# Kernel tuning notes

Measured on AMD Instinct MI355X. Metric: run time of the kernel, lower is better.

The kernel has to match this reference:

```python
import jax, jax.numpy as jnp
import numpy as np

B = 64        # image batch
K = 8         # beam width k
T = 12        # program_len
H = 2048      # hd_sz
IN = 2048     # CNN feature size (in_sz)
D = 400       # num_draws (grammar size)
E = 128       # input_op_sz


def gumbel_log_survival(x):
    # log P(Gumbel > x), numerically stable (Kool et al.)
    y = jnp.exp(-x)
    return jnp.where(x >= 10.0, -x - y / 2 + y * y / 24,
                     jnp.log(-jnp.expm1(-jnp.exp(-jnp.minimum(x, 10.0)))))


def setup_inputs():
    key = jax.random.key(0)
    ks = jax.random.split(key, 14)
    s = lambda n: 1.0 / np.sqrt(n)
    f32 = jnp.float32
    return {
        "x_f": jax.random.normal(ks[0], (B, IN), f32),
        "x_f3_seq": jax.random.normal(ks[1], (T, B * K, IN), f32),
        "gumbel_u": jax.random.uniform(ks[2], (T, B * K, D), dtype=f32),
        "pop_syms": jax.random.randint(ks[3], (T, B * K), 0, D),
        "mask_table": jnp.where(jax.random.uniform(ks[4], (D, D)) < 0.25, -20.0, 0.0).astype(f32),
        "W_emb": jax.random.normal(ks[5], (E, D), f32) * s(D),
        "b_emb": jnp.zeros((E,), f32),
        "W_ih": jax.random.normal(ks[6], (4 * H, 2 * IN + E), f32) * s(2 * IN + E),
        "W_hh": jax.random.normal(ks[7], (4 * H, H), f32) * s(H),
        "b_ih": jnp.zeros((4 * H,), f32),
        "b_hh": jnp.zeros((4 * H,), f32),
        "W_fc1": jax.random.normal(ks[8], (H, H), f32) * s(H),
        "b_fc1": jnp.zeros((H,), f32),
        "W_out": jax.random.normal(ks[9], (D, H), f32) * s(H),
        "b_out": jnp.zeros((D,), f32),
    }


def _forward(x_f, x_f3_seq, gumbel_u, mask_table, W_emb, b_emb, W_ih, W_hh,
             b_ih, b_hh, W_fc1, b_fc1, W_out, b_out, pop_syms):
    BK = B * K
    sg = jax.lax.stop_gradient
    xf = jnp.tile(x_f, (K, 1))                        # [BK, IN] beams share CNN feature
    mask_bin = (mask_table == 0).astype(jnp.float32)  # mask.get_mask
    rows = jnp.arange(BK)
    base = jnp.tile(jnp.arange(B), K)
    bias = b_ih + b_hh

    def step(carry, xs):
        h, c, G, logp, samples, outs, ent, entp, wpq, lgp = carry
        t, pop, xf3, u = xs
        # one-hot(pop) -> dense+relu op embedding
        emb = jax.nn.relu(jax.nn.one_hot(pop, D, dtype=jnp.float32) @ W_emb.T + b_emb)
        # single-step LSTM (torch gate order i,f,g,o); dropout is identity (eval)
        z = jnp.concatenate([xf, emb, xf3], axis=1) @ W_ih.T + h @ W_hh.T + bias
        i_, f_, g_, o_ = jnp.split(z, 4, axis=-1)
        c2 = jax.nn.sigmoid(f_) * c + jax.nn.sigmoid(i_) * jnp.tanh(g_)
        h2 = jax.nn.sigmoid(o_) * jnp.tanh(c2)
        hd = jax.nn.relu(h2 @ W_fc1.T + b_fc1)
        logits = hd @ W_out.T + b_out + mask_table[pop]
        logp_tok = jax.nn.log_softmax(logits, axis=1)
        probs = jnp.exp(logp_tok)
        greedy = jnp.argmax(probs, axis=1)

        # Gumbel-with-maximum + top-k beam step (all detached, as in torch)
        gum = -jnp.log(-jnp.log(jnp.clip(u, 1e-9, 1.0 - 1e-9)))
        g_phi = sg(logp_tok) + sg(logp) + gum
        Z = jnp.max(g_phi, axis=1, keepdims=True)
        v = G - g_phi + jnp.log1p(-jnp.exp(g_phi - Z))
        g = sg(G - jax.nn.relu(v) - jnp.log1p(jnp.exp(-jnp.abs(v))))
        # beams are laid out in blocks of B rows; gather per-image candidates
        g2 = g.reshape(K, B, D).transpose(1, 0, 2).reshape(B, K * D)
        g_val, idx = jax.lax.top_k(g2, K)
        is0 = t == 0
        order = jnp.where(is0, rows, (idx // D).T.reshape(BK) * B + base)
        sample = jnp.where(is0, greedy, (idx % D).T.reshape(BK))
        G2 = jnp.where(is0, G, g_val.T.reshape(BK, 1))

        out_lp = logp_tok[order]
        out_pr = probs[order]
        sel = jnp.take_along_axis(out_lp, sample[:, None], axis=1)  # [BK,1]
        logp2 = jnp.where(is0, logp[order], logp[order] + sel)
        samples2 = samples[order].at[:, t].set(sample.astype(jnp.float32))
        outs2 = outs[order].at[:, t].set(sel[:, 0])

        # importance-weighted entropy estimate (active for t > 0)
        ent_full = jnp.sum(out_lp * out_pr * mask_bin[pop[order]], axis=1)
        g_k = sg(jnp.tile(g_val[:, -1:], (1, K - 1)))
        phi_k = logp2[:, 0].reshape(K, B).T[:, :K - 1]
        w = sg(jnp.exp(phi_k - gumbel_log_survival(g_k - sg(phi_k))))
        ent_mat = ent_full.reshape(K, B).T[:, :K - 1]
        upd = jnp.sum(w * ent_mat, axis=1)
        ent2 = ent + jnp.where(is0, 0.0, upd / jnp.sum(w, axis=1))
        entp2 = entp + jnp.where(is0, 0.0, upd)
        wpq2 = jnp.where(is0, wpq, w)
        lgp2 = jnp.where(is0, lgp, phi_k)
        new_carry = (h2[order], c2[order], G2, logp2, samples2, outs2,
                     ent2, entp2, wpq2, lgp2)
        return new_carry, None

    f32 = jnp.float32
    carry0 = (jnp.zeros((BK, H), f32), jnp.zeros((BK, H), f32),
              jnp.zeros((BK, 1), f32), jnp.zeros((BK, 1), f32),
              jnp.zeros((BK, T), f32), jnp.zeros((BK, T), f32),
              jnp.zeros((B,), f32), jnp.zeros((B,), f32),
              jnp.zeros((B, K - 1), f32), jnp.zeros((B, K - 1), f32))
    xs = (jnp.arange(T), pop_syms, x_f3_seq, gumbel_u)
    (_, _, _, _, samples, outs, ent, entp, wpq, lgp), _ = jax.lax.scan(step, carry0, xs)
    # drop last beam, lay out [B, (K-1)*T] as in the torch split/cat epilogue
    take = lambda a: a.reshape(K, B, T)[:K - 1].transpose(1, 0, 2).reshape(B, (K - 1) * T)
    return take(outs), take(samples), ent, wpq, lgp


def reference(x_f, x_f3_seq, gumbel_u, pop_syms, mask_table, W_emb, b_emb, W_ih,
              W_hh, b_ih, b_hh, W_fc1, b_fc1, W_out, b_out):
    return _forward(x_f, x_f3_seq, gumbel_u, mask_table, W_emb, b_emb, W_ih, W_hh,
                    b_ih, b_hh, W_fc1, b_fc1, W_out, b_out, pop_syms)
```

## Files before the change

### kernel.cpp

```cpp
#include <hip/hip_runtime.h>
#include <math.h>


#define BB   64
#define KK   8
#define TT   12
#define HH   2048
#define DD   400
#define EE   128
#define BKR  512
#define G4   8192

static const size_t OFF_STATE = 0;
static const size_t OFF_H     = 114688;
static const size_t OFF_C     = 4308992;
static const size_t ZERO_END  = 8503296;
static const size_t OFF_Z     = 8503296;
static const size_t OFF_H2    = 42057728;
static const size_t OFF_C2    = 46252032;
static const size_t OFF_HD    = 50446336;
static const size_t OFF_EMB   = 54640640;
static const size_t OFF_XFW   = 54902784;
static const size_t OFF_BIAS  = 56999936;
static const size_t OFF_LPT   = 57032704;
static const size_t OFF_GMAT  = 58671104;
static const size_t OFF_INTS  = 60309504;
static const size_t WS_TOTAL  = 60313600;

#define SI_G    0
#define SI_LOGP 512
#define SI_SAMP 1024
#define SI_OUTS 7168
#define SI_ENT  13312
#define SI_WPQ  13376
#define SI_LGP  13824

using half8  = __attribute__((ext_vector_type(8))) _Float16;
using floatx4 = __attribute__((ext_vector_type(4))) float;

__global__ __launch_bounds__(256, 2)
void ij_gemm_f16x3(const float* __restrict__ A0, const float* __restrict__ A1,
                   const float* __restrict__ A2, int kA1, int kA2,
                   int lda0, int lda1, int lda2,
                   const float* __restrict__ B0, const float* __restrict__ B1,
                   int kB1, int ldb0, int ldb1,
                   float* __restrict__ C, int N, int Klen)
{
    __shared__ half8 lds[2048];

    const int tid = threadIdx.x;
    const int n0  = blockIdx.x * 128;
    const int m0  = blockIdx.y * 128;
    const int kstart = blockIdx.z * Klen;
    const int nch = Klen / 32;
    float* Cout = C + (size_t)blockIdx.z * ((size_t)512 * (size_t)N);

    const int wid    = tid >> 6;
    const int wave_m = wid & 1;
    const int wave_n = wid >> 1;
    const int lane   = tid & 63;
    const int lo16   = lane & 15;
    const int oq     = lane >> 4;
    const int laneSlot = oq * 16 + ((lo16 + 4 * oq) & 15);

    const int st_o   = tid & 3;
    const int st_row0 = tid >> 2;
    const int st_slot = ((st_row0 & 15) + 4 * st_o) & 15;

    float4 pfA[2][2], pfB[2][2];

    auto loadGlobals = [&](int c) {
        const int kb = kstart + c * 32;
#pragma unroll
        for (int i = 0; i < 2; ++i) {
            const int row = st_row0 + i * 64;
            const int kc  = kb + st_o * 8;
            const float* ap; int ao, ld;
            if (kc < kA1)      { ap = A0; ao = kc;       ld = lda0; }
            else if (kc < kA2) { ap = A1; ao = kc - kA1; ld = lda1; }
            else               { ap = A2; ao = kc - kA2; ld = lda2; }
            const float* p = ap + (size_t)(m0 + row) * ld + ao;
            pfA[i][0] = *(const float4*)(p);
            pfA[i][1] = *(const float4*)(p + 4);
            const int bn = n0 + row;
            const float* bp; int bo, bld;
            if (kc < kB1) { bp = B0; bo = kc;       bld = ldb0; }
            else          { bp = B1; bo = kc - kB1; bld = ldb1; }
            if (bn < N) {
                const float* q = bp + (size_t)bn * bld + bo;
                pfB[i][0] = *(const float4*)(q);
                pfB[i][1] = *(const float4*)(q + 4);
            } else {
                pfB[i][0] = make_float4(0.f,0.f,0.f,0.f);
                pfB[i][1] = make_float4(0.f,0.f,0.f,0.f);
            }
        }
    };

    auto writeLDS = [&]() {
#pragma unroll
        for (int i = 0; i < 2; ++i) {
            const int row = st_row0 + i * 64;
            const int mt  = row >> 4;
            const int idx = mt * 64 + st_o * 16 + (((row & 15) + 4 * st_o) & 15);
            {
                float x[8] = {pfA[i][0].x, pfA[i][0].y, pfA[i][0].z, pfA[i][0].w,
                              pfA[i][1].x, pfA[i][1].y, pfA[i][1].z, pfA[i][1].w};
                half8 hi8, lo8;
#pragma unroll
                for (int j = 0; j < 8; ++j) {
                    _Float16 h = (_Float16)x[j];
                    hi8[j] = h;
                    lo8[j] = (_Float16)((x[j] - (float)h) * 2048.0f);
                }
                lds[idx]       = hi8;
                lds[512 + idx] = lo8;
            }
            {
                float x[8] = {pfB[i][0].x, pfB[i][0].y, pfB[i][0].z, pfB[i][0].w,
                              pfB[i][1].x, pfB[i][1].y, pfB[i][1].z, pfB[i][1].w};
                half8 hi8, lo8;
#pragma unroll
                for (int j = 0; j < 8; ++j) {
                    _Float16 h = (_Float16)x[j];
                    hi8[j] = h;
                    lo8[j] = (_Float16)((x[j] - (float)h) * 2048.0f);
                }
                lds[1024 + idx] = hi8;
                lds[1536 + idx] = lo8;
            }
        }
    };

    floatx4 acc1[4][4], acc2[4][4];
#pragma unroll
    for (int i = 0; i < 4; ++i)
#pragma unroll
        for (int j = 0; j < 4; ++j) { acc1[i][j] = (floatx4)0.f; acc2[i][j] = (floatx4)0.f; }

    loadGlobals(0);
    for (int c = 0; c < nch; ++c) {
        __syncthreads();
        writeLDS();
        __syncthreads();
        if (c + 1 < nch) loadGlobals(c + 1);

        half8 Ahi[4], Alo[4];
#pragma unroll
        for (int mt = 0; mt < 4; ++mt) {
            const int amt = wave_m * 4 + mt;
            Ahi[mt] = lds[amt * 64 + laneSlot];
            Alo[mt] = lds[512 + amt * 64 + laneSlot];
        }
#pragma unroll
        for (int nt = 0; nt < 4; ++nt) {
            const int bnt = wave_n * 4 + nt;
            half8 Bhi = lds[1024 + bnt * 64 + laneSlot];
            half8 Blo = lds[1536 + bnt * 64 + laneSlot];
#pragma unroll
            for (int mt = 0; mt < 4; ++mt) {
                acc1[mt][nt] = __builtin_amdgcn_mfma_f32_16x16x32_f16(Ahi[mt], Bhi, acc1[mt][nt], 0, 0, 0);
                acc2[mt][nt] = __builtin_amdgcn_mfma_f32_16x16x32_f16(Ahi[mt], Blo, acc2[mt][nt], 0, 0, 0);
                acc2[mt][nt] = __builtin_amdgcn_mfma_f32_16x16x32_f16(Alo[mt], Bhi, acc2[mt][nt], 0, 0, 0);
            }
        }
    }

    const float s = 1.0f / 2048.0f;
#pragma unroll
    for (int mt = 0; mt < 4; ++mt) {
        const int rbase = m0 + wave_m * 64 + mt * 16 + oq * 4;
#pragma unroll
        for (int nt = 0; nt < 4; ++nt) {
            const int col = n0 + wave_n * 64 + nt * 16 + lo16;
            if (col >= N) continue;
#pragma unroll
            for (int v = 0; v < 4; ++v) {
                float val = acc1[mt][nt][v] + acc2[mt][nt][v] * s;
                Cout[(size_t)(rbase + v) * N + col] = val;
            }
        }
    }
}

#define FBM 128
#define FBN 64
#define FBK 16

__global__ __launch_bounds__(256, 2)
void ij_gemm_f32(const float* __restrict__ A0, const float* __restrict__ A1,
                 const float* __restrict__ A2, int kA1, int kA2,
                 int lda0, int lda1, int lda2,
                 const float* __restrict__ B0, const float* __restrict__ B1,
                 int kB1, int ldb0, int ldb1,
                 float* __restrict__ C, int M, int N, int Klen)
{
    __shared__ float As[2][FBK][FBM];
    __shared__ float Bs[2][FBK][FBN];

    const int tid = threadIdx.x;
    const int tx  = tid & 15;
    const int ty  = tid >> 4;
    const int n0  = blockIdx.x * FBN;
    const int m0  = blockIdx.y * FBM;
    const int kstart = blockIdx.z * Klen;
    const int nch = Klen / FBK;
    float* Cout = C + (size_t)blockIdx.z * ((size_t)M * (size_t)N);

    const int srow = tid >> 2;
    const int kq   = tid & 3;

    float4 aR0, aR1, bR;

    auto loadChunk = [&](int kb0) {
        const int kc = kb0 + kq * 4;
        const float* ap; int ao, ld;
        if (kc < kA1)      { ap = A0; ao = kc;       ld = lda0; }
        else if (kc < kA2) { ap = A1; ao = kc - kA1; ld = lda1; }
        else               { ap = A2; ao = kc - kA2; ld = lda2; }
        const int r0 = m0 + srow, r1 = r0 + 64;
        aR0 = (r0 < M) ? *(const float4*)(ap + (size_t)r0 * ld + ao)
                       : make_float4(0.f, 0.f, 0.f, 0.f);
        aR1 = (r1 < M) ? *(const float4*)(ap + (size_t)r1 * ld + ao)
                       : make_float4(0.f, 0.f, 0.f, 0.f);
        const float* bp; int bo, bld;
        if (kc < kB1) { bp = B0; bo = kc;       bld = ldb0; }
        else          { bp = B1; bo = kc - kB1; bld = ldb1; }
        const int bn = n0 + srow;
        bR = (bn < N) ? *(const float4*)(bp + (size_t)bn * bld + bo)
                      : make_float4(0.f, 0.f, 0.f, 0.f);
    };
    auto storeChunk = [&](int bsel) {
        const int k4 = kq * 4;
        As[bsel][k4+0][srow]      = aR0.x;
        As[bsel][k4+1][srow]      = aR0.y;
        As[bsel][k4+2][srow]      = aR0.z;
        As[bsel][k4+3][srow]      = aR0.w;
        As[bsel][k4+0][srow + 64] = aR1.x;
        As[bsel][k4+1][srow + 64] = aR1.y;
        As[bsel][k4+2][srow + 64] = aR1.z;
        As[bsel][k4+3][srow + 64] = aR1.w;
        Bs[bsel][k4+0][srow]      = bR.x;
        Bs[bsel][k4+1][srow]      = bR.y;
        Bs[bsel][k4+2][srow]      = bR.z;
        Bs[bsel][k4+3][srow]      = bR.w;
    };

    float acc[8][4];
#pragma unroll
    for (int i = 0; i < 8; ++i)
#pragma unroll
        for (int j = 0; j < 4; ++j) acc[i][j] = 0.f;

    loadChunk(kstart);
    storeChunk(0);
    __syncthreads();
    int bsel = 0;
    for (int c = 0; c < nch; ++c) {
        if (c + 1 < nch) loadChunk(kstart + (c + 1) * FBK);
#pragma unroll
        for (int kkk = 0; kkk < FBK; ++kkk) {
            float a[8], b[4];
            const float4 av0 = *(const float4*)&As[bsel][kkk][ty * 8];
            const float4 av1 = *(const float4*)&As[bsel][kkk][ty * 8 + 4];
            a[0]=av0.x; a[1]=av0.y; a[2]=av0.z; a[3]=av0.w;
            a[4]=av1.x; a[5]=av1.y; a[6]=av1.z; a[7]=av1.w;
            const float2 bv0 = *(const float2*)&Bs[bsel][kkk][tx * 2];
            const float2 bv1 = *(const float2*)&Bs[bsel][kkk][tx * 2 + 32];
            b[0]=bv0.x; b[1]=bv0.y; b[2]=bv1.x; b[3]=bv1.y;
#pragma unroll
            for (int i = 0; i < 8; ++i)
#pragma unroll
                for (int j = 0; j < 4; ++j)
                    acc[i][j] = fmaf(a[i], b[j], acc[i][j]);
        }
        if (c + 1 < nch) storeChunk(bsel ^ 1);
        __syncthreads();
        bsel ^= 1;
    }

#pragma unroll
    for (int i = 0; i < 8; ++i) {
        const int row = m0 + ty * 8 + i;
        if (row >= M) continue;
        const size_t rbase = (size_t)row * N;
#pragma unroll
        for (int g = 0; g < 2; ++g) {
            const int col = n0 + tx * 2 + g * 32;
            if (col + 1 < N) {
                float2 st; st.x = acc[i][g*2+0]; st.y = acc[i][g*2+1];
                *(float2*)(Cout + rbase + col) = st;
            } else if (col < N) {
                Cout[rbase + col] = acc[i][g*2+0];
            }
        }
    }
}

__global__ void ij_bias_kernel(const float* __restrict__ b_ih, const float* __restrict__ b_hh,
                               float* __restrict__ bias)
{
    int i = blockIdx.x * 256 + threadIdx.x;
    if (i < G4) bias[i] = b_ih[i] + b_hh[i];
}

__global__ void ij_emb_kernel(const float* __restrict__ W_emb, const float* __restrict__ b_emb,
                              const int* __restrict__ pop_t, float* __restrict__ emb)
{
    int i = blockIdx.x * 256 + threadIdx.x;
    if (i >= BKR * EE) return;
    int r = i >> 7, e = i & 127;
    float v = W_emb[e * DD + pop_t[r]] + b_emb[e];
    emb[i] = v > 0.f ? v : 0.f;
}

__global__ void ij_lstm_kernel(const float* __restrict__ z0, const float* __restrict__ z1,
                               const float* __restrict__ xfw, const float* __restrict__ bias,
                               const float* __restrict__ c,
                               float* __restrict__ h2, float* __restrict__ c2)
{
    int i = blockIdx.x * 256 + threadIdx.x;
    if (i >= BKR * HH) return;
    int r = i >> 11, hh = i & 2047;
    const size_t zb = (size_t)r * G4;
    const float* xw = xfw + (size_t)(r & 63) * G4;
    float iv = z0[zb + hh]        + z1[zb + hh]        + xw[hh]        + bias[hh];
    float fv = z0[zb + HH + hh]   + z1[zb + HH + hh]   + xw[HH + hh]   + bias[HH + hh];
    float gv = z0[zb + 2*HH + hh] + z1[zb + 2*HH + hh] + xw[2*HH + hh] + bias[2*HH + hh];
    float ov = z0[zb + 3*HH + hh] + z1[zb + 3*HH + hh] + xw[3*HH + hh] + bias[3*HH + hh];
    float si = 1.f / (1.f + expf(-iv));
    float sf = 1.f / (1.f + expf(-fv));
    float so = 1.f / (1.f + expf(-ov));
    float cv = sf * c[i] + si * tanhf(gv);
    c2[i] = cv;
    h2[i] = so * tanhf(cv);
}

__global__ void ij_reduce_fc1_kernel(const float* __restrict__ part, const float* __restrict__ b_fc1,
                                     float* __restrict__ hd)
{
    int i = blockIdx.x * 256 + threadIdx.x;
    if (i >= BKR * HH) return;
    float v = part[i] + part[i + 1048576] + part[i + 2097152] + part[i + 3145728]
            + b_fc1[i & 2047];
    hd[i] = v > 0.f ? v : 0.f;
}

__global__ void ij_reduce_xfw_kernel(const float* __restrict__ part, float* __restrict__ xfw)
{
    int i = blockIdx.x * 256 + threadIdx.x;
    if (i >= BB * G4) return;
    xfw[i] = part[i] + part[i + 524288] + part[i + 1048576] + part[i + 1572864];
}

__global__ __launch_bounds__(256)
void ij_softmax_g_kernel(const float* __restrict__ part, const float* __restrict__ b_out,
                         const float* __restrict__ mask_table, const int* __restrict__ pop_t,
                         const float* __restrict__ gum_t, const double* __restrict__ G,
                         const double* __restrict__ logp,
                         double* __restrict__ logp_tok, double* __restrict__ gmat,
                         int* __restrict__ greedy)
{
    const int r = blockIdx.x, tid = threadIdx.x;
    __shared__ double sred[256];
    __shared__ int    sidx[256];
    __shared__ double sbc[2];

    const int pop = pop_t[r];
    const int j0 = tid, j1 = tid + 256;
    double lg0 = -INFINITY, lg1 = -INFINITY;
    if (j0 < DD) {
        double v = (double)b_out[j0] + (double)mask_table[pop * DD + j0];
#pragma unroll
        for (int s = 0; s < 16; ++s) v += (double)part[(size_t)s * (BKR*DD) + (size_t)r * DD + j0];
        lg0 = v;
    }
    if (j1 < DD) {
        double v = (double)b_out[j1] + (double)mask_table[pop * DD + j1];
#pragma unroll
        for (int s = 0; s < 16; ++s) v += (double)part[(size_t)s * (BKR*DD) + (size_t)r * DD + j1];
        lg1 = v;
    }
    double mv = lg0; int mi = j0;
    if (lg1 > mv) { mv = lg1; mi = j1; }
    sred[tid] = mv; sidx[tid] = mi;
    __syncthreads();
    for (int off = 128; off > 0; off >>= 1) {
        if (tid < off) {
            double ov = sred[tid+off]; int oi = sidx[tid+off];
            if (ov > sred[tid] || (ov == sred[tid] && oi < sidx[tid])) { sred[tid] = ov; sidx[tid] = oi; }
        }
        __syncthreads();
    }
    if (tid == 0) { sbc[0] = sred[0]; greedy[r] = sidx[0]; }
    __syncthreads();
    const double rowmax = sbc[0];

    double es = 0.0;
    if (j0 < DD) es += exp(lg0 - rowmax);
    if (j1 < DD) es += exp(lg1 - rowmax);
    __syncthreads();
    sred[tid] = es;
    __syncthreads();
    for (int off = 128; off > 0; off >>= 1) {
        if (tid < off) sred[tid] += sred[tid+off];
        __syncthreads();
    }
    if (tid == 0) sbc[1] = log(sred[0]);
    __syncthreads();
    const double lse = sbc[1];
    const double lpr = logp[r], Gr = G[r];

    double gp0 = -INFINITY, gp1 = -INFINITY;
    if (j0 < DD) {
        double lt = lg0 - rowmax - lse;
        logp_tok[(size_t)r * DD + j0] = lt;
        double u = (double)gum_t[(size_t)r * DD + j0];
        u = fmin(fmax(u, 1e-9), 1.0 - 1e-9);
        gp0 = lt + lpr + (-log(-log(u)));
    }
    if (j1 < DD) {
        double lt = lg1 - rowmax - lse;
        logp_tok[(size_t)r * DD + j1] = lt;
        double u = (double)gum_t[(size_t)r * DD + j1];
        u = fmin(fmax(u, 1e-9), 1.0 - 1e-9);
        gp1 = lt + lpr + (-log(-log(u)));
    }
    __syncthreads();
    sred[tid] = fmax(gp0, gp1);
    __syncthreads();
    for (int off = 128; off > 0; off >>= 1) {
        if (tid < off) sred[tid] = fmax(sred[tid], sred[tid+off]);
        __syncthreads();
    }
    const double Z = sred[0];
    if (j0 < DD) {
        double v = Gr - gp0 + log1p(-exp(gp0 - Z));
        gmat[(size_t)r * DD + j0] = Gr - fmax(v, 0.0) - log1p(exp(-fabs(v)));
    }
    if (j1 < DD) {
        double v = Gr - gp1 + log1p(-exp(gp1 - Z));
        gmat[(size_t)r * DD + j1] = Gr - fmax(v, 0.0) - log1p(exp(-fabs(v)));
    }
}

__global__ __launch_bounds__(256)
void ij_beam_kernel(const double* __restrict__ gmat, const double* __restrict__ logp_tok,
                    const int* __restrict__ greedy, const int* __restrict__ pop_t,
                    const float* __restrict__ mask_table,
                    double* __restrict__ G, double* __restrict__ logp,
                    double* __restrict__ samples, double* __restrict__ outs,
                    double* __restrict__ entacc, double* __restrict__ wpq,
                    double* __restrict__ lgp_o, int* __restrict__ order_g, int t)
{
    const int b = blockIdx.x, tid = threadIdx.x;
    __shared__ double sv[256];
    __shared__ int    si2[256];
    __shared__ double gval8[8];
    __shared__ int    gidx8[8];
    __shared__ int    ord8[8], smp8[8];
    __shared__ double lp28[8], sel8[8], Gn8[8];
    __shared__ double oldS[8][TT], oldO[8][TT];
    __shared__ double efull[8];

    if (t > 0) {
        for (int pass = 0; pass < 8; ++pass) {
            double bv = -INFINITY; int bi = 0x7fffffff;
            for (int cand = tid; cand < KK * DD; cand += 256) {
                bool used = false;
                for (int p = 0; p < pass; ++p) used |= (gidx8[p] == cand);
                if (used) continue;
                int kb2 = cand / DD, d = cand - kb2 * DD;
                double v = gmat[(size_t)(kb2 * BB + b) * DD + d];
                if (v > bv || (v == bv && cand < bi)) { bv = v; bi = cand; }
            }
            sv[tid] = bv; si2[tid] = bi;
            __syncthreads();
            for (int off = 128; off > 0; off >>= 1) {
                if (tid < off) {
                    double ov = sv[tid+off]; int oi = si2[tid+off];
                    if (ov > sv[tid] || (ov == sv[tid] && oi < si2[tid])) { sv[tid] = ov; si2[tid] = oi; }
                }
                __syncthreads();
            }
            if (tid == 0) { gval8[pass] = sv[0]; gidx8[pass] = si2[0]; }
            __syncthreads();
        }
    }

    if (tid < 8) {
        const int s = tid, rp = s * BB + b;
        int ord, smp; double Gn;
        if (t == 0) { ord = rp; smp = greedy[rp]; Gn = G[rp]; }
        else {
            int idx = gidx8[s]; int kb2 = idx / DD;
            ord = kb2 * BB + b; smp = idx - kb2 * DD; Gn = gval8[s];
        }
        ord8[s] = ord; smp8[s] = smp; Gn8[s] = Gn;
        double sel = logp_tok[(size_t)ord * DD + smp];
        double lp2 = (t == 0) ? logp[ord] : logp[ord] + sel;
        sel8[s] = sel; lp28[s] = lp2;
    }
    __syncthreads();
    if (tid < 8 * TT) {
        int s = tid / TT, ttc = tid - s * TT;
        oldS[s][ttc] = samples[ord8[s] * TT + ttc];
        oldO[s][ttc] = outs[ord8[s] * TT + ttc];
    }
    __syncthreads();
    if (tid < 8 * TT) {
        int s = tid / TT, ttc = tid - s * TT;
        int rp = s * BB + b;
        samples[rp * TT + ttc] = (ttc == t) ? (double)smp8[s] : oldS[s][ttc];
        outs[rp * TT + ttc]    = (ttc == t) ? sel8[s]         : oldO[s][ttc];
    }
    if (tid >= 96 && tid < 104) {
        int s = tid - 96, rp = s * BB + b;
        G[rp]       = Gn8[s];
        logp[rp]    = lp28[s];
        order_g[rp] = ord8[s];
    }

    if (t > 0) {
        for (int s = 0; s < KK - 1; ++s) {
            const int ord = ord8[s];
            const double* lrow = logp_tok + (size_t)ord * DD;
            const float*  mrow = mask_table + (size_t)pop_t[ord] * DD;
            double acc = 0.0;
            for (int j = tid; j < DD; j += 256) {
                double lp_ = lrow[j];
                if (mrow[j] == 0.0f) acc += lp_ * exp(lp_);
            }
            __syncthreads();
            sv[tid] = acc;
            __syncthreads();
            for (int off = 128; off > 0; off >>= 1) {
                if (tid < off) sv[tid] += sv[tid+off];
                __syncthreads();
            }
            if (tid == 0) efull[s] = sv[0];
            __syncthreads();
        }
        if (tid == 0) {
            const double gk = gval8[7];
            double sw = 0.0, swe = 0.0;
            for (int s = 0; s < KK - 1; ++s) {
                double phi = lp28[s];
                double x = gk - phi;
                double y = exp(-x);
                double gls;
                if (x >= 10.0) gls = -x - y * 0.5 + y * y * (1.0 / 24.0);
                else           gls = log(-expm1(-exp(-fmin(x, 10.0))));
                double w = exp(phi - gls);
                wpq[b * (KK-1) + s]   = w;
                lgp_o[b * (KK-1) + s] = phi;
                sw += w; swe += w * efull[s];
            }
            entacc[b] += swe / sw;
        }
    }
}

__global__ void ij_permute_kernel(const float* __restrict__ h2, const float* __restrict__ c2,
                                  const int* __restrict__ order_g,
                                  float* __restrict__ h, float* __restrict__ c)
{
    int i = blockIdx.x * 256 + threadIdx.x;
    if (i >= BKR * HH) return;
    int r = i >> 11, j = i & 2047;
    int o = order_g[r];
    h[i] = h2[(size_t)o * HH + j];
    c[i] = c2[(size_t)o * HH + j];
}

__global__ void ij_final_kernel(const double* __restrict__ outs, const double* __restrict__ samples,
                                const double* __restrict__ entacc, const double* __restrict__ wpq,
                                const double* __restrict__ lgp_o, float* __restrict__ out)
{
    int i = blockIdx.x * 256 + threadIdx.x;
    if (i < 5376) {
        int bb = i / 84, rest = i - bb * 84;
        int s = rest / TT, ttc = rest - s * TT;
        size_t src = (size_t)(s * BB + bb) * TT + ttc;
        out[i]        = (float)outs[src];
        out[5376 + i] = (float)samples[src];
    } else if (i < 5440) {
        out[10752 + (i - 5376)] = (float)entacc[i - 5376];
    } else if (i < 5888) {
        int q = i - 5440; out[10816 + q] = (float)wpq[q];
    } else if (i < 6336) {
        int q = i - 5888; out[11264 + q] = (float)lgp_o[q];
    }
}

extern "C" void kernel_launch(void* const* d_in, const int* in_sizes, int n_in,
                              void* d_out, int out_size, void* d_ws, size_t ws_size,
                              hipStream_t stream)
{
    const float* x_f   = (const float*)d_in[0];
    const float* x_f3  = (const float*)d_in[1];
    const float* gum   = (const float*)d_in[2];
    const int*   pop   = (const int*)d_in[3];
    const float* mask  = (const float*)d_in[4];
    const float* W_emb = (const float*)d_in[5];
    const float* b_emb = (const float*)d_in[6];
    const float* W_ih  = (const float*)d_in[7];
    const float* W_hh  = (const float*)d_in[8];
    const float* b_ih  = (const float*)d_in[9];
    const float* b_hh  = (const float*)d_in[10];
    const float* W_fc1 = (const float*)d_in[11];
    const float* b_fc1 = (const float*)d_in[12];
    const float* W_out = (const float*)d_in[13];
    const float* b_out = (const float*)d_in[14];
    float* out = (float*)d_out;
    char*  ws  = (char*)d_ws;

    if (ws_size < WS_TOTAL) return;

    double* STATE = (double*)(ws + OFF_STATE);
    double* Gv    = STATE + SI_G;
    double* LOGP  = STATE + SI_LOGP;
    double* SAMP  = STATE + SI_SAMP;
    double* OUTS  = STATE + SI_OUTS;
    double* ENT   = STATE + SI_ENT;
    double* WPQ   = STATE + SI_WPQ;
    double* LGP   = STATE + SI_LGP;
    float*  H     = (float*)(ws + OFF_H);
    float*  Cc    = (float*)(ws + OFF_C);
    float*  Z     = (float*)(ws + OFF_Z);
    float*  Z1    = Z + (size_t)BKR * G4;
    float*  H2    = (float*)(ws + OFF_H2);
    float*  C2    = (float*)(ws + OFF_C2);
    float*  HD    = (float*)(ws + OFF_HD);
    float*  EMB   = (float*)(ws + OFF_EMB);
    float*  XFW   = (float*)(ws + OFF_XFW);
    float*  BIAS  = (float*)(ws + OFF_BIAS);
    double* LPT   = (double*)(ws + OFF_LPT);
    double* GMAT  = (double*)(ws + OFF_GMAT);
    int*    ORDER = (int*)(ws + OFF_INTS);
    int*    GREEDY= ORDER + 512;

    hipMemsetAsync(ws, 0, ZERO_END, stream);
    ij_bias_kernel<<<32, 256, 0, stream>>>(b_ih, b_hh, BIAS);

    ij_gemm_f32<<<dim3(128, 1, 4), 256, 0, stream>>>(
        x_f, nullptr, nullptr, 1 << 30, 1 << 30, 2048, 0, 0,
        W_ih, nullptr, 1 << 30, 4224, 0,
        Z, BB, G4, 512);
    ij_reduce_xfw_kernel<<<2048, 256, 0, stream>>>(Z, XFW);

    for (int t = 0; t < TT; ++t) {
        const int* pop_t = pop + t * BKR;
        ij_emb_kernel<<<256, 256, 0, stream>>>(W_emb, b_emb, pop_t, EMB);

        ij_gemm_f16x3<<<dim3(64, 4, 2), 256, 0, stream>>>(
            EMB, x_f3 + (size_t)t * BKR * 2048, H, 128, 2176, 128, 2048, 2048,
            W_ih + 2048, W_hh, 2176, 4224, 2048,
            Z, G4, 2112);

        ij_lstm_kernel<<<4096, 256, 0, stream>>>(Z, Z1, XFW, BIAS, Cc, H2, C2);

        ij_gemm_f16x3<<<dim3(16, 4, 4), 256, 0, stream>>>(
            H2, nullptr, nullptr, 1 << 30, 1 << 30, 2048, 0, 0,
            W_fc1, nullptr, 1 << 30, 2048, 0,
            Z, HH, 512);
        ij_reduce_fc1_kernel<<<4096, 256, 0, stream>>>(Z, b_fc1, HD);

        ij_gemm_f16x3<<<dim3(4, 4, 16), 256, 0, stream>>>(
            HD, nullptr, nullptr, 1 << 30, 1 << 30, 2048, 0, 0,
            W_out, nullptr, 1 << 30, 2048, 0,
            Z, DD, 128);

        ij_softmax_g_kernel<<<512, 256, 0, stream>>>(
            Z, b_out, mask, pop_t, gum + (size_t)t * BKR * DD,
            Gv, LOGP, LPT, GMAT, GREEDY);

        ij_beam_kernel<<<64, 256, 0, stream>>>(
            GMAT, LPT, GREEDY, pop_t, mask,
            Gv, LOGP, SAMP, OUTS, ENT, WPQ, LGP, ORDER, t);

        ij_permute_kernel<<<4096, 256, 0, stream>>>(H2, C2, ORDER, H, Cc);
    }

    ij_final_kernel<<<25, 256, 0, stream>>>(OUTS, SAMP, ENT, WPQ, LGP, out);
    (void)in_sizes; (void)n_in; (void)out_size;
}
```

Measured before the change: 3.704 ms.

## Prepack fp16 hi/lo operands into MFMA tile layout and stream via LDS-direct loads

Adds a new execution path that converts the weights (W_ih, W_hh, W_fc1, W_out) and the per-step CNN features into split fp16 hi/lo pairs once per call. They are stored in a tiled layout that matches the MFMA fragment order. Producer kernels (embedding, LSTM cell, fc1 reduce, beam permute) now emit their outputs directly in this packed format. A new GEMM kernel then fills LDS with global_load_lds and does no per-tile fp32-to-fp16 splitting, removing conversion ALU work and register staging from the inner loop. In exchange, the path needs a much larger workspace and an up-front packing pass over all weights on every call, and it only runs when the provided workspace is big enough.

```diff
diff --git a/kernel.cpp b/kernel.cpp
--- a/kernel.cpp
+++ b/kernel.cpp
@@ -27,6 +27,27 @@
 static const size_t OFF_INTS  = 60309504;
 static const size_t WS_TOTAL  = 60313600;
 
+static const size_t NOFF_STATE = 0;
+static const size_t NOFF_C     = 114688;
+static const size_t NOFF_A16H  = 4308992;
+static const size_t NZERO_END  = 8503296;
+static const size_t NOFF_Z     = 8503296;
+static const size_t NOFF_H2    = 42057728;
+static const size_t NOFF_C2    = 46252032;
+static const size_t NOFF_XFW   = 50446336;
+static const size_t NOFF_BIAS  = 52543488;
+static const size_t NOFF_LPT   = 52576256;
+static const size_t NOFF_GMAT  = 54214656;
+static const size_t NOFF_INTS  = 55853056;
+static const size_t NOFF_A16E  = 55857152;
+static const size_t NOFF_A16X  = 56119296;
+static const size_t NOFF_A16F  = 106450944;
+static const size_t NOFF_A16D  = 110645248;
+static const size_t NOFF_B16G  = 114839552;
+static const size_t NOFF_B16F  = 253251584;
+static const size_t NOFF_B16O  = 270028800;
+static const size_t NWS_TOTAL  = 274223104;
+
 #define SI_G    0
 #define SI_LOGP 512
 #define SI_SAMP 1024
@@ -38,6 +59,300 @@
 using half8  = __attribute__((ext_vector_type(8))) _Float16;
 using floatx4 = __attribute__((ext_vector_type(4))) float;
 
+__device__ __forceinline__ void gload16(const void* g, void* l) {
+    __builtin_amdgcn_global_load_lds((__attribute__((address_space(1))) void*)g,
+                                     (__attribute__((address_space(3))) void*)l,
+                                     16, 0, 0);
+}
+
+__device__ __forceinline__ void split16v(float x, half8& hi, half8& lo, int j) {
+    _Float16 h = (_Float16)x;
+    hi[j] = h;
+    lo[j] = (_Float16)((x - (float)h) * 2048.0f);
+}
+
+__global__ __launch_bounds__(256, 2)
+void ij_gemm_pk(const half8* __restrict__ A0, const half8* __restrict__ A1,
+                const half8* __restrict__ A2, int cA1, int cA2,
+                int chA0, int chA1, int chA2,
+                const half8* __restrict__ Bt, int totB,
+                float* __restrict__ C, int N, int cpz)
+{
+    __shared__ half8 lds[2048];
+
+    const int tid  = threadIdx.x;
+    const int lane = tid & 63;
+    const int wid  = tid >> 6;
+    const int n0   = blockIdx.x * 128;
+    const int m0   = blockIdx.y * 128;
+    const int c0   = blockIdx.z * cpz;
+    float* Cout = C + (size_t)blockIdx.z * ((size_t)512 * (size_t)N);
+
+    const int wave_m = wid & 1;
+    const int wave_n = wid >> 1;
+    const int lo16 = lane & 15;
+    const int oq   = lane >> 4;
+
+    floatx4 acc1[4][4], acc2[4][4];
+#pragma unroll
+    for (int i = 0; i < 4; ++i)
+#pragma unroll
+        for (int j = 0; j < 4; ++j) { acc1[i][j] = (floatx4)0.f; acc2[i][j] = (floatx4)0.f; }
+
+    for (int c = 0; c < cpz; ++c) {
+        const int ca = c0 + c;
+        __syncthreads();
+        if (wid < 2) {
+            const half8* ap; int cl, st;
+            if (ca < cA1)      { ap = A0; cl = ca;       st = chA0; }
+            else if (ca < cA2) { ap = A1; cl = ca - cA1; st = chA1; }
+            else               { ap = A2; cl = ca - cA2; st = chA2; }
+            const half8* src = ap + ((size_t)blockIdx.y * st + cl) * 1024 + lane;
+#pragma unroll
+            for (int j = 0; j < 8; ++j) {
+                const int un = (wid * 8 + j) * 64;
+                gload16(src + un, &lds[un]);
+            }
+        } else {
+            const half8* src = Bt + ((size_t)blockIdx.x * totB + ca) * 1024 + lane;
+#pragma unroll
+            for (int j = 0; j < 8; ++j) {
+                const int un = ((wid - 2) * 8 + j) * 64;
+                gload16(src + un, &lds[1024 + un]);
+            }
+        }
+        __syncthreads();
+
+        half8 Ahi[4], Alo[4];
+#pragma unroll
+        for (int mt = 0; mt < 4; ++mt) {
+            const int amt = wave_m * 4 + mt;
+            Ahi[mt] = lds[amt * 64 + lane];
+            Alo[mt] = lds[512 + amt * 64 + lane];
+        }
+#pragma unroll
+        for (int nt = 0; nt < 4; ++nt) {
+            const int bnt = wave_n * 4 + nt;
+            half8 Bhi = lds[1024 + bnt * 64 + lane];
+            half8 Blo = lds[1536 + bnt * 64 + lane];
+#pragma unroll
+            for (int mt = 0; mt < 4; ++mt) {
+                acc1[mt][nt] = __builtin_amdgcn_mfma_f32_16x16x32_f16(Ahi[mt], Bhi, acc1[mt][nt], 0, 0, 0);
+                acc2[mt][nt] = __builtin_amdgcn_mfma_f32_16x16x32_f16(Ahi[mt], Blo, acc2[mt][nt], 0, 0, 0);
+                acc2[mt][nt] = __builtin_amdgcn_mfma_f32_16x16x32_f16(Alo[mt], Bhi, acc2[mt][nt], 0, 0, 0);
+            }
+        }
+    }
+
+    const float s = 1.0f / 2048.0f;
+#pragma unroll
+    for (int mt = 0; mt < 4; ++mt) {
+        const int rbase = m0 + wave_m * 64 + mt * 16 + oq * 4;
+#pragma unroll
+        for (int nt = 0; nt < 4; ++nt) {
+            const int col = n0 + wave_n * 64 + nt * 16 + lo16;
+            if (col >= N) continue;
+#pragma unroll
+            for (int v = 0; v < 4; ++v) {
+                float val = acc1[mt][nt][v] + acc2[mt][nt][v] * s;
+                Cout[(size_t)(rbase + v) * N + col] = val;
+            }
+        }
+    }
+}
+
+__global__ void ij_pack_w(const float* __restrict__ S0, const float* __restrict__ S1,
+                          int kS1, int ld0, int ld1,
+                          int Nw, int tot_ch, int total, half8* __restrict__ out)
+{
+    int gid = blockIdx.x * 256 + threadIdx.x;
+    if (gid >= total) return;
+    const int kpr  = tot_ch * 4;
+    const int koct = gid % kpr;
+    const int row  = gid / kpr;
+    const int c  = koct >> 2;
+    const int oqq = koct & 3;
+    const int k0 = koct * 8;
+    const int nb = row >> 7, mt = (row >> 4) & 7, lo16 = row & 15;
+    const int u  = mt * 64 + oqq * 16 + lo16;
+
+    half8 hi8, lo8;
+    if (row < Nw) {
+        const float* sp; int ko, ld;
+        if (k0 < kS1) { sp = S0; ko = k0;       ld = ld0; }
+        else          { sp = S1; ko = k0 - kS1; ld = ld1; }
+        const float4 a = *(const float4*)(sp + (size_t)row * ld + ko);
+        const float4 b = *(const float4*)(sp + (size_t)row * ld + ko + 4);
+        float x[8] = {a.x, a.y, a.z, a.w, b.x, b.y, b.z, b.w};
+#pragma unroll
+        for (int j = 0; j < 8; ++j) split16v(x[j], hi8, lo8, j);
+    } else {
+#pragma unroll
+        for (int j = 0; j < 8; ++j) { hi8[j] = (_Float16)0.f; lo8[j] = (_Float16)0.f; }
+    }
+    const size_t base = ((size_t)nb * tot_ch + c) * 1024;
+    out[base + u]       = hi8;
+    out[base + 512 + u] = lo8;
+}
+
+__global__ void ij_pack_emb(const float* __restrict__ W_emb, const float* __restrict__ b_emb,
+                            const int* __restrict__ pop_t, half8* __restrict__ out)
+{
+    int gid = blockIdx.x * 256 + threadIdx.x;
+    if (gid >= BKR * 16) return;
+    const int koct = gid & 15;
+    const int row  = gid >> 4;
+    const int c  = koct >> 2;
+    const int oqq = koct & 3;
+    const int k0 = koct * 8;
+    const int nb = row >> 7, mt = (row >> 4) & 7, lo16 = row & 15;
+    const int u  = mt * 64 + oqq * 16 + lo16;
+    const int p  = pop_t[row];
+
+    half8 hi8, lo8;
+#pragma unroll
+    for (int e = 0; e < 8; ++e) {
+        const int col = k0 + e;
+        float v = W_emb[col * DD + p] + b_emb[col];
+        v = v > 0.f ? v : 0.f;
+        split16v(v, hi8, lo8, e);
+    }
+    const size_t base = ((size_t)nb * 4 + c) * 1024;
+    out[base + u]       = hi8;
+    out[base + 512 + u] = lo8;
+}
+
+__global__ void ij_lstm_pk(const float* __restrict__ z0, const float* __restrict__ z1,
+                           const float* __restrict__ xfw, const float* __restrict__ bias,
+                           const float* __restrict__ c,
+                           float* __restrict__ h2, float* __restrict__ c2,
+                           half8* __restrict__ a16f)
+{
+    int gid = blockIdx.x * 256 + threadIdx.x;
+    if (gid >= BKR * 256) return;
+    const int r   = gid >> 8;
+    const int oct = gid & 255;
+    const int hh0 = oct * 8;
+    const size_t zb = (size_t)r * G4;
+    const float* xw = xfw + (size_t)(r & 63) * G4;
+
+    float zg[4][8];
+#pragma unroll
+    for (int g = 0; g < 4; ++g) {
+        const int base = g * HH + hh0;
+        const float4 a0 = *(const float4*)(z0 + zb + base);
+        const float4 a1 = *(const float4*)(z0 + zb + base + 4);
+        const float4 b0 = *(const float4*)(z1 + zb + base);
+        const float4 b1 = *(const float4*)(z1 + zb + base + 4);
+        const float4 w0 = *(const float4*)(xw + base);
+        const float4 w1 = *(const float4*)(xw + base + 4);
+        const float4 s0 = *(const float4*)(bias + base);
+        const float4 s1 = *(const float4*)(bias + base + 4);
+        zg[g][0] = a0.x + b0.x + w0.x + s0.x;  zg[g][1] = a0.y + b0.y + w0.y + s0.y;
+        zg[g][2] = a0.z + b0.z + w0.z + s0.z;  zg[g][3] = a0.w + b0.w + w0.w + s0.w;
+        zg[g][4] = a1.x + b1.x + w1.x + s1.x;  zg[g][5] = a1.y + b1.y + w1.y + s1.y;
+        zg[g][6] = a1.z + b1.z + w1.z + s1.z;  zg[g][7] = a1.w + b1.w + w1.w + s1.w;
+    }
+    const size_t ib = (size_t)r * HH + hh0;
+    const float4 cp0 = *(const float4*)(c + ib);
+    const float4 cp1 = *(const float4*)(c + ib + 4);
+    float cprev[8] = {cp0.x, cp0.y, cp0.z, cp0.w, cp1.x, cp1.y, cp1.z, cp1.w};
+
+    float h2v[8], c2v[8];
+#pragma unroll
+    for (int e = 0; e < 8; ++e) {
+        float si = 1.f / (1.f + expf(-zg[0][e]));
+        float sf = 1.f / (1.f + expf(-zg[1][e]));
+        float gt = tanhf(zg[2][e]);
+        float so = 1.f / (1.f + expf(-zg[3][e]));
+        float cv = sf * cprev[e] + si * gt;
+        c2v[e] = cv;
+        h2v[e] = so * tanhf(cv);
+    }
+    *(float4*)(c2 + ib)     = make_float4(c2v[0], c2v[1], c2v[2], c2v[3]);
+    *(float4*)(c2 + ib + 4) = make_float4(c2v[4], c2v[5], c2v[6], c2v[7]);
+    *(float4*)(h2 + ib)     = make_float4(h2v[0], h2v[1], h2v[2], h2v[3]);
+    *(float4*)(h2 + ib + 4) = make_float4(h2v[4], h2v[5], h2v[6], h2v[7]);
+
+    half8 hi8, lo8;
+#pragma unroll
+    for (int e = 0; e < 8; ++e) split16v(h2v[e], hi8, lo8, e);
+    const int cch = oct >> 2, oqq = oct & 3;
+    const int mt = (r >> 4) & 7, lo16 = r & 15;
+    const size_t base = ((size_t)(r >> 7) * 64 + cch) * 1024;
+    const int u = mt * 64 + oqq * 16 + lo16;
+    a16f[base + u]       = hi8;
+    a16f[base + 512 + u] = lo8;
+}
+
+__global__ void ij_reduce_fc1_pk(const float* __restrict__ part, const float* __restrict__ b_fc1,
+                                 half8* __restrict__ a16d)
+{
+    int gid = blockIdx.x * 256 + threadIdx.x;
+    if (gid >= BKR * 256) return;
+    const int r   = gid >> 8;
+    const int oct = gid & 255;
+    const int hh0 = oct * 8;
+    const size_t i = (size_t)r * HH + hh0;
+
+    float v[8];
+    {
+        const float4 b0 = *(const float4*)(b_fc1 + hh0);
+        const float4 b1 = *(const float4*)(b_fc1 + hh0 + 4);
+        v[0]=b0.x; v[1]=b0.y; v[2]=b0.z; v[3]=b0.w; v[4]=b1.x; v[5]=b1.y; v[6]=b1.z; v[7]=b1.w;
+    }
+#pragma unroll
+    for (int s = 0; s < 8; ++s) {
+        const float4 p0 = *(const float4*)(part + (size_t)s * 1048576 + i);
+        const float4 p1 = *(const float4*)(part + (size_t)s * 1048576 + i + 4);
+        v[0]+=p0.x; v[1]+=p0.y; v[2]+=p0.z; v[3]+=p0.w; v[4]+=p1.x; v[5]+=p1.y; v[6]+=p1.z; v[7]+=p1.w;
+    }
+    half8 hi8, lo8;
+#pragma unroll
+    for (int e = 0; e < 8; ++e) {
+        float x = v[e] > 0.f ? v[e] : 0.f;
+        split16v(x, hi8, lo8, e);
+    }
+    const int cch = oct >> 2, oqq = oct & 3;
+    const int mt = (r >> 4) & 7, lo16 = r & 15;
+    const size_t base = ((size_t)(r >> 7) * 64 + cch) * 1024;
+    const int u = mt * 64 + oqq * 16 + lo16;
+    a16d[base + u]       = hi8;
+    a16d[base + 512 + u] = lo8;
+}
+
+__global__ void ij_permute_pk(const float* __restrict__ h2, const float* __restrict__ c2,
+                              const int* __restrict__ order_g,
+                              float* __restrict__ c, half8* __restrict__ a16h)
+{
+    int gid = blockIdx.x * 256 + threadIdx.x;
+    if (gid >= BKR * 256) return;
+    const int r   = gid >> 8;
+    const int oct = gid & 255;
+    const int hh0 = oct * 8;
+    const int o   = order_g[r];
+    const size_t so_ = (size_t)o * HH + hh0;
+    const size_t di  = (size_t)r * HH + hh0;
+
+    const float4 cc0 = *(const float4*)(c2 + so_);
+    const float4 cc1 = *(const float4*)(c2 + so_ + 4);
+    *(float4*)(c + di)     = cc0;
+    *(float4*)(c + di + 4) = cc1;
+
+    const float4 hh0v = *(const float4*)(h2 + so_);
+    const float4 hh1v = *(const float4*)(h2 + so_ + 4);
+    float hv[8] = {hh0v.x, hh0v.y, hh0v.z, hh0v.w, hh1v.x, hh1v.y, hh1v.z, hh1v.w};
+    half8 hi8, lo8;
+#pragma unroll
+    for (int e = 0; e < 8; ++e) split16v(hv[e], hi8, lo8, e);
+    const int cch = oct >> 2, oqq = oct & 3;
+    const int mt = (r >> 4) & 7, lo16 = r & 15;
+    const size_t base = ((size_t)(r >> 7) * 64 + cch) * 1024;
+    const int u = mt * 64 + oqq * 16 + lo16;
+    a16h[base + u]       = hi8;
+    a16h[base + 512 + u] = lo8;
+}
+
 __global__ __launch_bounds__(256, 2)
 void ij_gemm_f16x3(const float* __restrict__ A0, const float* __restrict__ A1,
                    const float* __restrict__ A2, int kA1, int kA2,
@@ -65,7 +380,6 @@
 
     const int st_o   = tid & 3;
     const int st_row0 = tid >> 2;
-    const int st_slot = ((st_row0 & 15) + 4 * st_o) & 15;
 
     float4 pfA[2][2], pfB[2][2];
 
@@ -108,11 +422,7 @@
                               pfA[i][1].x, pfA[i][1].y, pfA[i][1].z, pfA[i][1].w};
                 half8 hi8, lo8;
 #pragma unroll
-                for (int j = 0; j < 8; ++j) {
-                    _Float16 h = (_Float16)x[j];
-                    hi8[j] = h;
-                    lo8[j] = (_Float16)((x[j] - (float)h) * 2048.0f);
-                }
+                for (int j = 0; j < 8; ++j) split16v(x[j], hi8, lo8, j);
                 lds[idx]       = hi8;
                 lds[512 + idx] = lo8;
             }
@@ -121,11 +431,7 @@
                               pfB[i][1].x, pfB[i][1].y, pfB[i][1].z, pfB[i][1].w};
                 half8 hi8, lo8;
 #pragma unroll
-                for (int j = 0; j < 8; ++j) {
-                    _Float16 h = (_Float16)x[j];
-                    hi8[j] = h;
-                    lo8[j] = (_Float16)((x[j] - (float)h) * 2048.0f);
-                }
+                for (int j = 0; j < 8; ++j) split16v(x[j], hi8, lo8, j);
                 lds[1024 + idx] = hi8;
                 lds[1536 + idx] = lo8;
             }
@@ -615,6 +921,96 @@
     float* out = (float*)d_out;
     char*  ws  = (char*)d_ws;
 
+    if (ws_size >= NWS_TOTAL) {
+        double* STATE = (double*)(ws + NOFF_STATE);
+        double* Gv    = STATE + SI_G;
+        double* LOGP  = STATE + SI_LOGP;
+        double* SAMP  = STATE + SI_SAMP;
+        double* OUTS  = STATE + SI_OUTS;
+        double* ENT   = STATE + SI_ENT;
+        double* WPQ   = STATE + SI_WPQ;
+        double* LGP   = STATE + SI_LGP;
+        float*  Cc    = (float*)(ws + NOFF_C);
+        half8*  A16H  = (half8*)(ws + NOFF_A16H);
+        float*  Z     = (float*)(ws + NOFF_Z);
+        float*  Z1    = Z + (size_t)BKR * G4;
+        float*  H2    = (float*)(ws + NOFF_H2);
+        float*  C2    = (float*)(ws + NOFF_C2);
+        float*  XFW   = (float*)(ws + NOFF_XFW);
+        float*  BIAS  = (float*)(ws + NOFF_BIAS);
+        double* LPT   = (double*)(ws + NOFF_LPT);
+        double* GMAT  = (double*)(ws + NOFF_GMAT);
+        int*    ORDER = (int*)(ws + NOFF_INTS);
+        int*    GREEDY= ORDER + 512;
+        half8*  A16E  = (half8*)(ws + NOFF_A16E);
+        half8*  A16X  = (half8*)(ws + NOFF_A16X);
+        half8*  A16F  = (half8*)(ws + NOFF_A16F);
+        half8*  A16D  = (half8*)(ws + NOFF_A16D);
+        half8*  B16G  = (half8*)(ws + NOFF_B16G);
+        half8*  B16F  = (half8*)(ws + NOFF_B16F);
+        half8*  B16O  = (half8*)(ws + NOFF_B16O);
+
+        hipMemsetAsync(ws, 0, NZERO_END, stream);
+        ij_bias_kernel<<<32, 256, 0, stream>>>(b_ih, b_hh, BIAS);
+
+        {
+            int tot = 8192 * 132 * 4;
+            ij_pack_w<<<(tot + 255) / 256, 256, 0, stream>>>(
+                W_ih + 2048, W_hh, 2176, 4224, 2048, 8192, 132, tot, B16G);
+            tot = 2048 * 64 * 4;
+            ij_pack_w<<<(tot + 255) / 256, 256, 0, stream>>>(
+                W_fc1, nullptr, 1 << 30, 2048, 0, 2048, 64, tot, B16F);
+            tot = 512 * 64 * 4;
+            ij_pack_w<<<(tot + 255) / 256, 256, 0, stream>>>(
+                W_out, nullptr, 1 << 30, 2048, 0, 400, 64, tot, B16O);
+            tot = 512 * 64 * 4;
+            for (int t = 0; t < TT; ++t)
+                ij_pack_w<<<(tot + 255) / 256, 256, 0, stream>>>(
+                    x_f3 + (size_t)t * BKR * 2048, nullptr, 1 << 30, 2048, 0,
+                    512, 64, tot, A16X + (size_t)t * 262144);
+        }
+
+        ij_gemm_f32<<<dim3(128, 1, 4), 256, 0, stream>>>(
+            x_f, nullptr, nullptr, 1 << 30, 1 << 30, 2048, 0, 0,
+            W_ih, nullptr, 1 << 30, 4224, 0,
+            Z, BB, G4, 512);
+        ij_reduce_xfw_kernel<<<2048, 256, 0, stream>>>(Z, XFW);
+
+        for (int t = 0; t < TT; ++t) {
+            const int* pop_t = pop + t * BKR;
+            ij_pack_emb<<<32, 256, 0, stream>>>(W_emb, b_emb, pop_t, A16E);
+
+            ij_gemm_pk<<<dim3(64, 4, 2), 256, 0, stream>>>(
+                A16E, A16X + (size_t)t * 262144, A16H, 4, 68, 4, 64, 64,
+                B16G, 132, Z, G4, 66);
+
+            ij_lstm_pk<<<512, 256, 0, stream>>>(Z, Z1, XFW, BIAS, Cc, H2, C2, A16F);
+
+            ij_gemm_pk<<<dim3(16, 4, 8), 256, 0, stream>>>(
+                A16F, A16F, A16F, 1 << 30, 1 << 30, 64, 64, 64,
+                B16F, 64, Z, HH, 8);
+            ij_reduce_fc1_pk<<<512, 256, 0, stream>>>(Z, b_fc1, A16D);
+
+            ij_gemm_pk<<<dim3(4, 4, 16), 256, 0, stream>>>(
+                A16D, A16D, A16D, 1 << 30, 1 << 30, 64, 64, 64,
+                B16O, 64, Z, DD, 4);
+
+            ij_softmax_g_kernel<<<512, 256, 0, stream>>>(
+                Z, b_out, mask, pop_t, gum + (size_t)t * BKR * DD,
+                Gv, LOGP, LPT, GMAT, GREEDY);
+
+            ij_beam_kernel<<<64, 256, 0, stream>>>(
+                GMAT, LPT, GREEDY, pop_t, mask,
+                Gv, LOGP, SAMP, OUTS, ENT, WPQ, LGP, ORDER, t);
+
+            ij_permute_pk<<<512, 256, 0, stream>>>(H2, C2, ORDER, Cc, A16H);
+        }
+
+        ij_final_kernel<<<25, 256, 0, stream>>>(OUTS, SAMP, ENT, WPQ, LGP, out);
+        (void)in_sizes; (void)n_in; (void)out_size;
+        return;
+    }
+
     if (ws_size < WS_TOTAL) return;
 
     double* STATE = (double*)(ws + OFF_STATE);
```

Result: faster. 3.334 ms (-10.0%).
